# Optimization experiments

Hardware: AMD Instinct MI355X
Metric: run time of the kernel (lower is better)

## Reference

```python
import jax, jax.numpy as jnp
import numpy as np

B, S, DM, TD, H, HD = 2, 2048, 1024, 1024, 16, 64


def setup_inputs() -> dict:
    key = jax.random.key(0)
    k1, k2, k3, k4 = jax.random.split(key, 4)
    query = jax.random.normal(k1, (B, S, DM), dtype=jnp.float32)
    # fused QKV projection weight (nn.Linear weight layout: [out, in]) and output proj
    W_in = jax.random.normal(k2, (3 * TD, DM), dtype=jnp.float32) * 0.02
    W_out = jax.random.normal(k3, (DM, TD), dtype=jnp.float32) * 0.02
    # standard RoPE tables, broadcastable against [B, H, S, HD]
    inv_freq = 1.0 / (10000.0 ** (jnp.arange(0, HD, 2, dtype=jnp.float32) / HD))
    t = jnp.arange(S, dtype=jnp.float32)
    freqs = jnp.outer(t, inv_freq)                      # [S, HD/2]
    emb = jnp.concatenate([freqs, freqs], axis=-1)      # [S, HD]
    sin_q = jnp.sin(emb)[None, None]                    # [1,1,S,HD]
    cos_q = jnp.cos(emb)[None, None]
    # padding mask over keys: first length[b] positions valid (>= S/2 so no NaN rows)
    lengths = jax.random.randint(k4, (B,), S // 2, S + 1)
    attn_mask = jnp.arange(S)[None, :] < lengths[:, None]  # [B, S] bool
    return {"query": query, "W_in": W_in, "W_out": W_out,
            "sin_q": sin_q, "cos_q": cos_q, "attn_mask": attn_mask}


def _rotate_half(x):
    x1, x2 = jnp.split(x, 2, axis=-1)
    return jnp.concatenate([-x2, x1], axis=-1)


def reference(query, W_in, W_out, sin_q, cos_q, attn_mask):
    # fused QKV projection (proj_in, bias=False)
    qkv = query @ W_in.T                                # [B, S, 3*TD]
    q, k, v = jnp.split(qkv, 3, axis=-1)
    to_heads = lambda x: x.reshape(B, S, H, HD).transpose(0, 2, 1, 3)  # [B,H,S,HD]
    q, k, v = to_heads(q), to_heads(k), to_heads(v)
    # RoPE (prefix = 0 since sin covers full sequence)
    q = q * cos_q + _rotate_half(q) * sin_q
    k = k * cos_q + _rotate_half(k) * sin_q
    # SDPA with padding-mask bias + causal mask
    scale = 1.0 / jnp.sqrt(jnp.float32(HD))
    scores = jnp.einsum('bhqd,bhkd->bhqk', q, k) * scale  # [B,H,S,S]
    causal = jnp.arange(S)[:, None] >= jnp.arange(S)[None, :]  # [S, S]
    mask = attn_mask[:, None, None, :] & causal[None, None]    # [B,1,S,S]
    scores = jnp.where(mask, scores, -jnp.inf)
    attn = jax.nn.softmax(scores, axis=-1)
    out = jnp.einsum('bhqk,bhkd->bhqd', attn, v)        # [B,H,S,HD]
    out = out.transpose(0, 2, 1, 3).reshape(B, S, TD)
    return out @ W_out.T                                 # [B, S, DM]
```

## Files before the change

### kernel.cpp

```cpp
#include <hip/hip_runtime.h>
#include <hip/hip_bf16.h>

#define B_ 2
#define S_ 2048
#define DM_ 1024
#define TD_ 1024
#define H_ 16
#define HD_ 64

using bf16 = __hip_bfloat16;
typedef __attribute__((ext_vector_type(8))) short s8v;
typedef __attribute__((ext_vector_type(4))) float f4v;

__device__ __forceinline__ f4v mfma_bf16(s8v a, s8v b, f4v c) {
    return __builtin_amdgcn_mfma_f32_16x16x32_bf16(a, b, c, 0, 0, 0);
}

__device__ __forceinline__ unsigned cvt_pk_bf16(float a, float b) {
    unsigned r;
    asm("v_cvt_pk_bf16_f32 %0, %1, %2" : "=v"(r) : "v"(a), "v"(b));
    return r;
}
__device__ __forceinline__ int2 pack4bf(float a, float b, float c, float d) {
    int2 r;
    r.x = (int)cvt_pk_bf16(a, b);
    r.y = (int)cvt_pk_bf16(c, d);
    return r;
}

__device__ __forceinline__ bool detect_f32(const unsigned int* __restrict__ cosw) {
    return (cosw[0] & 0xFFFFu) == 0u;
}

__device__ __forceinline__ void gload_lds16(const bf16* g, void* l) {
    __builtin_amdgcn_global_load_lds(
        (const __attribute__((address_space(1))) unsigned int*)(const void*)g,
        (__attribute__((address_space(3))) unsigned int*)l,
        16, 0, 0);
}

#define NQ_  (B_ * S_ * DM_)
#define NWI_ (3 * TD_ * DM_)
#define NWO_ (DM_ * TD_)
#define NCVT_BLOCKS ((NQ_ + NWI_ + NWO_) / 2048)

__global__ __launch_bounds__(256)
void prep_all(const void* __restrict__ q, const void* __restrict__ wi,
              const void* __restrict__ wo, bf16* __restrict__ dst,
              const void* __restrict__ mask, int* __restrict__ lengths,
              const unsigned int* __restrict__ cosw) {
    const int bid = blockIdx.x;
    if (bid < NCVT_BLOCKS) {
        const bool f32 = detect_f32(cosw);
        int i = (bid * 256 + threadIdx.x) * 8;
        const void* src; int off;
        if (i < NQ_)              { src = q;  off = i; }
        else if (i < NQ_ + NWI_)  { src = wi; off = i - NQ_; }
        else                      { src = wo; off = i - NQ_ - NWI_; }
        if (f32) {
            const float* p = (const float*)src + off;
            float4 x = *reinterpret_cast<const float4*>(p);
            float4 y = *reinterpret_cast<const float4*>(p + 4);
            union { unsigned u[4]; int4 v; } t;
            t.u[0] = cvt_pk_bf16(x.x, x.y);
            t.u[1] = cvt_pk_bf16(x.z, x.w);
            t.u[2] = cvt_pk_bf16(y.x, y.y);
            t.u[3] = cvt_pk_bf16(y.z, y.w);
            *reinterpret_cast<int4*>(dst + i) = t.v;
        } else {
            *reinterpret_cast<int4*>(dst + i) =
                *reinterpret_cast<const int4*>((const bf16*)src + off);
        }
        return;
    }
    int b = bid - NCVT_BLOCKS;
    unsigned int w0 = ((const unsigned int*)mask)[0];
    int enc;
    if (w0 == 1u) enc = 0;
    else if (w0 == 0x01010101u) enc = 1;
    else if (w0 == 0x3F803F80u) enc = 2;
    else enc = 3;
    int cnt = 0;
    for (int s = threadIdx.x; s < S_; s += 256) {
        int i = b * S_ + s;
        bool v;
        if (enc == 0)      v = ((const int*)mask)[i] != 0;
        else if (enc == 1) v = ((const unsigned char*)mask)[i] != 0;
        else if (enc == 2) v = ((const unsigned short*)mask)[i] != 0;
        else               v = ((const float*)mask)[i] != 0.f;
        cnt += v ? 1 : 0;
    }
    __shared__ int red[256];
    red[threadIdx.x] = cnt;
    __syncthreads();
    for (int off = 128; off > 0; off >>= 1) {
        if (threadIdx.x < off) red[threadIdx.x] += red[threadIdx.x + off];
        __syncthreads();
    }
    if (threadIdx.x == 0) lengths[b] = red[0];
}

__global__ __launch_bounds__(256, 4)
void gemm_out(const bf16* __restrict__ A, const bf16* __restrict__ Bm,
              void* __restrict__ C, int M, int N, int K,
              int c_dyn, const unsigned int* __restrict__ cosw) {
    __shared__ bf16 lds_a[128 * 64];
    __shared__ bf16 lds_b[64 * 64];

    const bool cf32 = c_dyn && detect_f32(cosw);

    const int t = threadIdx.x;
    const int wave = t >> 6, lane = t & 63;
    const int quad = lane >> 4, l16 = lane & 15;
    const int wm = wave >> 1, wn = wave & 1;
    const int bid = blockIdx.x;
    const int c = bid & 7, g = bid >> 3;
    const int m0 = (c * 4 + (g & 3)) * 128;
    const int n0 = (g >> 2) * 64;
    const int wuni = __builtin_amdgcn_readfirstlane(wave);

    f4v acc[4][2];
    #pragma unroll
    for (int i = 0; i < 4; i++)
        #pragma unroll
        for (int j = 0; j < 2; j++)
            acc[i][j] = f4v{0.f, 0.f, 0.f, 0.f};

    for (int k0 = 0; k0 < K; k0 += 64) {
        __syncthreads();
        #pragma unroll
        for (int i = 0; i < 4; i++) {
            int ci = i * 256 + t;
            int row = ci >> 3;
            int csrc = (ci & 7) ^ (row & 7);
            gload_lds16(A + (size_t)(m0 + row) * K + k0 + csrc * 8,
                        (char*)lds_a + i * 4096 + wuni * 1024);
        }
        #pragma unroll
        for (int i = 0; i < 2; i++) {
            int ci = i * 256 + t;
            int row = ci >> 3;
            int csrc = (ci & 7) ^ (row & 7);
            gload_lds16(Bm + (size_t)(n0 + row) * K + k0 + csrc * 8,
                        (char*)lds_b + i * 4096 + wuni * 1024);
        }
        __syncthreads();

        #pragma unroll
        for (int kk = 0; kk < 2; kk++) {
            s8v afr[4], bfr[2];
            #pragma unroll
            for (int mb = 0; mb < 4; mb++) {
                int r = wm * 64 + mb * 16 + l16;
                int ch = (kk * 4 + quad) ^ (l16 & 7);
                afr[mb] = *reinterpret_cast<const s8v*>(&lds_a[r * 64 + ch * 8]);
            }
            #pragma unroll
            for (int nb = 0; nb < 2; nb++) {
                int r = wn * 32 + nb * 16 + l16;
                int ch = (kk * 4 + quad) ^ (l16 & 7);
                bfr[nb] = *reinterpret_cast<const s8v*>(&lds_b[r * 64 + ch * 8]);
            }
            #pragma unroll
            for (int mb = 0; mb < 4; mb++)
                #pragma unroll
                for (int nb = 0; nb < 2; nb++)
                    acc[mb][nb] = mfma_bf16(bfr[nb], afr[mb], acc[mb][nb]);
        }
    }

    #pragma unroll
    for (int mb = 0; mb < 4; mb++) {
        int m = m0 + wm * 64 + mb * 16 + l16;
        #pragma unroll
        for (int nb = 0; nb < 2; nb++) {
            int n = n0 + wn * 32 + nb * 16 + quad * 4;
            f4v v = acc[mb][nb];
            if (cf32) {
                *reinterpret_cast<f4v*>(&((float*)C)[(size_t)m * N + n]) = v;
            } else {
                *reinterpret_cast<int2*>(&((bf16*)C)[(size_t)m * N + n]) =
                    pack4bf(v[0], v[1], v[2], v[3]);
            }
        }
    }
}

__global__ __launch_bounds__(256, 3)
void gemm_qkv(const bf16* __restrict__ A, const bf16* __restrict__ Bm,
              bf16* __restrict__ Qh, bf16* __restrict__ Kt, bf16* __restrict__ Vt,
              const void* __restrict__ sin_t, const void* __restrict__ cos_t) {
    __shared__ bf16 lds_a[128 * 64];
    __shared__ bf16 lds_b[128 * 64];

    const int t = threadIdx.x;
    const int wave = t >> 6, lane = t & 63;
    const int quad = lane >> 4, l16 = lane & 15;
    const int wm = wave >> 1, wn = wave & 1;
    const int bid = blockIdx.x;
    const int c = bid & 7, g = bid >> 3;
    const int m0 = (c * 4 + (g & 3)) * 128;
    const int n0 = (g >> 2) * 128;
    const int wuni = __builtin_amdgcn_readfirstlane(wave);

    f4v acc[4][4];
    #pragma unroll
    for (int i = 0; i < 4; i++)
        #pragma unroll
        for (int j = 0; j < 4; j++)
            acc[i][j] = f4v{0.f, 0.f, 0.f, 0.f};

    for (int k0 = 0; k0 < 1024; k0 += 64) {
        __syncthreads();
        #pragma unroll
        for (int i = 0; i < 4; i++) {
            int ci = i * 256 + t;
            int row = ci >> 3;
            int csrc = (ci & 7) ^ (row & 7);
            gload_lds16(A + (size_t)(m0 + row) * 1024 + k0 + csrc * 8,
                        (char*)lds_a + i * 4096 + wuni * 1024);
            gload_lds16(Bm + (size_t)(n0 + row) * 1024 + k0 + csrc * 8,
                        (char*)lds_b + i * 4096 + wuni * 1024);
        }
        __syncthreads();

        #pragma unroll
        for (int kk = 0; kk < 2; kk++) {
            s8v afr[4], bfr[4];
            #pragma unroll
            for (int mb = 0; mb < 4; mb++) {
                int r = wm * 64 + mb * 16 + l16;
                int ch = (kk * 4 + quad) ^ (l16 & 7);
                afr[mb] = *reinterpret_cast<const s8v*>(&lds_a[r * 64 + ch * 8]);
            }
            #pragma unroll
            for (int nb = 0; nb < 4; nb++) {
                int r = wn * 64 + nb * 16 + l16;
                int ch = (kk * 4 + quad) ^ (l16 & 7);
                bfr[nb] = *reinterpret_cast<const s8v*>(&lds_b[r * 64 + ch * 8]);
            }
            #pragma unroll
            for (int mb = 0; mb < 4; mb++)
                #pragma unroll
                for (int nb = 0; nb < 4; nb++)
                    acc[mb][nb] = mfma_bf16(bfr[nb], afr[mb], acc[mb][nb]);
        }
    }

    const int region = n0 >> 10;
    if (region < 2) {
        const bool f32 = detect_f32((const unsigned int*)cos_t);
        #pragma unroll
        for (int mb = 0; mb < 4; mb++) {
            const int m = m0 + wm * 64 + mb * 16 + l16;
            const int b = m >> 11, s = m & 2047;
            #pragma unroll
            for (int nb = 0; nb < 4; nb++) {
                const int n = n0 + wn * 64 + nb * 16 + quad * 4;
                const int d = n & 63;
                const int h = (n >> 6) & 15;
                const float sgn = (nb < 2) ? -1.f : 1.f;
                f4v v  = acc[mb][nb];
                f4v vp = acc[mb][nb ^ 2];
                float cs[4], sn[4];
                if (f32) {
                    float4 c4 = *reinterpret_cast<const float4*>(
                        (const float*)cos_t + s * 64 + d);
                    float4 s4 = *reinterpret_cast<const float4*>(
                        (const float*)sin_t + s * 64 + d);
                    cs[0] = c4.x; cs[1] = c4.y; cs[2] = c4.z; cs[3] = c4.w;
                    sn[0] = s4.x; sn[1] = s4.y; sn[2] = s4.z; sn[3] = s4.w;
                } else {
                    const bf16* cp = (const bf16*)cos_t + s * 64 + d;
                    const bf16* sp = (const bf16*)sin_t + s * 64 + d;
                    #pragma unroll
                    for (int r = 0; r < 4; r++) {
                        cs[r] = __bfloat162float(cp[r]);
                        sn[r] = __bfloat162float(sp[r]);
                    }
                }
                float y[4];
                #pragma unroll
                for (int r = 0; r < 4; r++)
                    y[r] = v[r] * cs[r] + sgn * vp[r] * sn[r];
                if (region == 0) {
                    size_t o = ((size_t)(b * H_ + h) * S_ + s) * 64 + d;
                    *reinterpret_cast<int2*>(&Qh[o]) =
                        pack4bf(y[0] * 0.180336880f, y[1] * 0.180336880f,
                                y[2] * 0.180336880f, y[3] * 0.180336880f);
                } else {
                    size_t kt = ((size_t)(b * H_ + h) * 32 + (s >> 6)) * 4096;
                    int dp = ((((d >> 3) ^ (s & 7)) << 3) | (d & 7));
                    *reinterpret_cast<int2*>(&Kt[kt + (s & 63) * 64 + dp]) =
                        pack4bf(y[0], y[1], y[2], y[3]);
                }
            }
        }
    } else {
        __syncthreads();
        bf16* half_w = (wm == 0) ? lds_a : lds_b;
        #pragma unroll
        for (int mb = 0; mb < 4; mb++) {
            const int slr = mb * 16 + l16;
            #pragma unroll
            for (int nb = 0; nb < 4; nb++) {
                const int nl = wn * 64 + nb * 16 + quad * 4;
                f4v v = acc[mb][nb];
                int off = (((nl >> 3) ^ (slr & 7)) << 3) | (nl & 7);
                *reinterpret_cast<int2*>(&half_w[slr * 128 + off]) =
                    pack4bf(v[0], v[1], v[2], v[3]);
            }
        }
        __syncthreads();
        const int b  = m0 >> 11;
        const int h0 = (n0 - 2048) >> 6;
        const int r0 = t & 7;
        #pragma unroll
        for (int i = 0; i < 8; i++) {
            int id  = i * 256 + t;
            int kc  = id & 7;
            int d   = (id >> 3) & 63;
            int sbl = (id >> 9) & 1;
            int hh  = id >> 10;
            int cb  = (hh << 3) | (d >> 3);
            const short* half_r = reinterpret_cast<const short*>(
                sbl ? lds_b : lds_a);
            union { short s_[8]; int4 v4; } u;
            #pragma unroll
            for (int j = 0; j < 8; j++) {
                int e   = (j + r0) & 7;
                int slr = kc * 8 + e;
                u.s_[e] = half_r[slr * 128 + (((cb ^ e) << 3) | (d & 7))];
            }
            size_t tb = ((size_t)(b * H_ + h0 + hh) * 32 +
                         ((m0 & 2047) >> 6) + sbl) * 4096;
            *reinterpret_cast<int4*>(&Vt[tb + d * 64 + ((kc ^ (d & 7)) << 3)]) = u.v4;
        }
    }
}

__global__ __launch_bounds__(256)
void attn_fused(const bf16* __restrict__ Qh, const bf16* __restrict__ Kt,
                const bf16* __restrict__ Vt, const int* __restrict__ lengths,
                bf16* __restrict__ out) {
    __shared__ bf16 k_buf[2 * 4096];
    __shared__ bf16 v_buf[2 * 4096];
    __shared__ bf16 lds_p[4 * 16 * 72];

    const int t = threadIdx.x, wave = t >> 6, lane = t & 63;
    const int quad = lane >> 4, l16 = lane & 15;
    const int bid = blockIdx.x;
    const int slot = bid >> 3;
    const int bh = (bid & 7) * 4 + (slot >> 4);
    const int p = slot & 15;
    const int b = bh >> 4, h = bh & 15;

    const size_t hb = (size_t)bh * S_ * 64;
    const bf16* Ktp = Kt + (size_t)bh * 32 * 4096;
    const bf16* Vtp = Vt + (size_t)bh * 32 * 4096;
    const int wuni = __builtin_amdgcn_readfirstlane(wave);
    int len_raw = lengths[b];
    const int len_b = len_raw < 1 ? 1 : (len_raw > S_ ? S_ : len_raw);
    const int nkt_len = (len_b + 63) >> 6;

    #pragma unroll
    for (int pass = 0; pass < 2; pass++) {
        const int qb = pass ? (31 - p) : p;
        const int qbase = qb * 64;
        const int qrow_g = qbase + wave * 16 + l16;
        const int kmax = (qrow_g < len_b - 1) ? qrow_g : (len_b - 1);

        s8v qf[2];
        {
            const bf16* qptr = Qh + hb + (size_t)qrow_g * 64 + quad * 8;
            qf[0] = *reinterpret_cast<const s8v*>(qptr);
            qf[1] = *reinterpret_cast<const s8v*>(qptr + 32);
        }

        f4v o_acc[4];
        #pragma unroll
        for (int a = 0; a < 4; a++) o_acc[a] = f4v{0.f, 0.f, 0.f, 0.f};
        float l_sum = 0.f;

        const int nkt = (qb + 1) < nkt_len ? (qb + 1) : nkt_len;

        f4v s_prev[4];
        auto process_tile = [&](int pt, const bf16* vb) {
            const int pbase = pt * 64;
            const bool tail = (pt == qb) || (pbase + 64 > len_b);
            #pragma unroll
            for (int a = 0; a < 4; a++) {
                float e0[4];
                #pragma unroll
                for (int r = 0; r < 4; r++) {
                    float e = __builtin_amdgcn_exp2f(s_prev[a][r]);
                    if (tail) {
                        int key = pbase + a * 16 + quad * 4 + r;
                        e = (key <= kmax) ? e : 0.f;
                    }
                    e0[r] = e;
                    l_sum += e;
                }
                *reinterpret_cast<int2*>(
                    &lds_p[(wave * 16 + l16) * 72 + a * 16 + quad * 4]) =
                    pack4bf(e0[0], e0[1], e0[2], e0[3]);
            }
            asm volatile("s_waitcnt lgkmcnt(0)" ::: "memory");
            __builtin_amdgcn_s_setprio(1);
            #pragma unroll
            for (int kk = 0; kk < 2; kk++) {
                s8v pf = *reinterpret_cast<const s8v*>(
                    &lds_p[(wave * 16 + l16) * 72 + kk * 32 + quad * 8]);
                #pragma unroll
                for (int a = 0; a < 4; a++) {
                    int ch = (kk * 4 + quad) ^ (l16 & 7);
                    s8v vf = *reinterpret_cast<const s8v*>(
                        &vb[(a * 16 + l16) * 64 + ch * 8]);
                    o_acc[a] = mfma_bf16(vf, pf, o_acc[a]);
                }
            }
            __builtin_amdgcn_s_setprio(0);
        };

        #pragma unroll
        for (int i = 0; i < 2; i++) {
            int ci = i * 256 + t;
            gload_lds16(Ktp + ci * 8, (char*)k_buf + i * 4096 + wuni * 1024);
        }
        __syncthreads();

        for (int kt = 0; kt < nkt; kt++) {
            const int cur = kt & 1;
            {
                const bf16* vst = Vtp + (size_t)kt * 4096;
                #pragma unroll
                for (int i = 0; i < 2; i++) {
                    int ci = i * 256 + t;
                    gload_lds16(vst + ci * 8,
                                (char*)v_buf + cur * 8192 + i * 4096 + wuni * 1024);
                }
            }
            if (kt + 1 < nkt) {
                const bf16* kst = Ktp + (size_t)(kt + 1) * 4096;
                #pragma unroll
                for (int i = 0; i < 2; i++) {
                    int ci = i * 256 + t;
                    gload_lds16(kst + ci * 8,
                                (char*)k_buf + (cur ^ 1) * 8192 + i * 4096 + wuni * 1024);
                }
            }

            const bf16* kb = k_buf + cur * 4096;
            f4v s_acc[4];
            #pragma unroll
            for (int a = 0; a < 4; a++) s_acc[a] = f4v{0.f, 0.f, 0.f, 0.f};
            __builtin_amdgcn_s_setprio(1);
            #pragma unroll
            for (int kk = 0; kk < 2; kk++) {
                #pragma unroll
                for (int a = 0; a < 4; a++) {
                    int ch = (kk * 4 + quad) ^ (l16 & 7);
                    s8v kf = *reinterpret_cast<const s8v*>(
                        &kb[(a * 16 + l16) * 64 + ch * 8]);
                    s_acc[a] = mfma_bf16(kf, qf[kk], s_acc[a]);
                }
            }
            __builtin_amdgcn_s_setprio(0);

            if (kt > 0) process_tile(kt - 1, v_buf + ((kt - 1) & 1) * 4096);

            #pragma unroll
            for (int a = 0; a < 4; a++) s_prev[a] = s_acc[a];

            __syncthreads();
        }
        process_tile(nkt - 1, v_buf + ((nkt - 1) & 1) * 4096);

        l_sum += __shfl_xor(l_sum, 16);
        l_sum += __shfl_xor(l_sum, 32);
        float inv_l = 1.f / l_sum;
        size_t orow = ((size_t)(b * S_ + qrow_g)) * TD_ + h * 64;
        #pragma unroll
        for (int a = 0; a < 4; a++) {
            *reinterpret_cast<int2*>(&out[orow + a * 16 + quad * 4]) =
                pack4bf(o_acc[a][0] * inv_l, o_acc[a][1] * inv_l,
                        o_acc[a][2] * inv_l, o_acc[a][3] * inv_l);
        }
    }
}

extern "C" void kernel_launch(void* const* d_in, const int* in_sizes, int n_in,
                              void* d_out, int out_size, void* d_ws, size_t ws_size,
                              hipStream_t stream) {
    const void* query = d_in[0];
    const void* W_in  = d_in[1];
    const void* W_out = d_in[2];
    const void* sin_q = d_in[3];
    const void* cos_q = d_in[4];
    const void* mask  = d_in[5];
    const unsigned int* cosw = (const unsigned int*)cos_q;

    const size_t nQ  = NQ_;
    const size_t nWi = NWI_;
    const size_t nWo = NWO_;

    bf16* base = (bf16*)d_ws;
    bf16* attn = base;
    bf16* Vt   = base + (size_t)4096 * 1024;
    bf16* Qh   = base + (size_t)2 * 4096 * 1024;
    bf16* Kt   = Qh + nQ;
    bf16* qbf  = Kt + nQ;
    bf16* wibf = qbf + nQ;
    bf16* wobf = wibf + nWi;
    int* lengths = (int*)(wobf + nWo);

    prep_all<<<NCVT_BLOCKS + B_, 256, 0, stream>>>(
        query, W_in, W_out, qbf, mask, lengths, cosw);

    gemm_qkv<<<768, 256, 0, stream>>>(qbf, wibf, Qh, Kt, Vt, sin_q, cos_q);

    attn_fused<<<512, 256, 0, stream>>>(Qh, Kt, Vt, lengths, attn);

    gemm_out<<<512, 256, 0, stream>>>(attn, wobf, d_out, 4096, 1024, 1024, 1, cosw);
}
```

Measured before the change: 177.2 us.

## Triple-buffer K/V tiles with prefetch distance two and partial vmcnt waits

Replaces the double-buffered K/V staging in the attention kernel with three-slot ring buffers. K is now prefetched two tiles ahead and V one tile ahead. The full __syncthreads waits become s_waitcnt vmcnt(N) plus s_barrier, so loads still in flight can stay outstanding across the barrier. This aims to hide global-to-LDS latency better, at the cost of more LDS per block (possible occupancy loss), modulo-3 index arithmetic, and fragile vmcnt counting.

```diff
diff --git a/kernel.cpp b/kernel.cpp
--- a/kernel.cpp
+++ b/kernel.cpp
@@ -343,8 +343,8 @@
 void attn_fused(const bf16* __restrict__ Qh, const bf16* __restrict__ Kt,
                 const bf16* __restrict__ Vt, const int* __restrict__ lengths,
                 bf16* __restrict__ out) {
-    __shared__ bf16 k_buf[2 * 4096];
-    __shared__ bf16 v_buf[2 * 4096];
+    __shared__ bf16 k_buf[3 * 4096];
+    __shared__ bf16 v_buf[3 * 4096];
     __shared__ bf16 lds_p[4 * 16 * 72];
 
     const int t = threadIdx.x, wave = t >> 6, lane = t & 63;
@@ -366,8 +366,7 @@
     #pragma unroll
     for (int pass = 0; pass < 2; pass++) {
         const int qb = pass ? (31 - p) : p;
-        const int qbase = qb * 64;
-        const int qrow_g = qbase + wave * 16 + l16;
+        const int qrow_g = qb * 64 + wave * 16 + l16;
         const int kmax = (qrow_g < len_b - 1) ? qrow_g : (len_b - 1);
 
         s8v qf[2];
@@ -422,35 +421,46 @@
             __builtin_amdgcn_s_setprio(0);
         };
 
-        #pragma unroll
-        for (int i = 0; i < 2; i++) {
-            int ci = i * 256 + t;
-            gload_lds16(Ktp + ci * 8, (char*)k_buf + i * 4096 + wuni * 1024);
-        }
-        __syncthreads();
+        __syncthreads();
+
+        #pragma unroll
+        for (int i = 0; i < 2; i++)
+            gload_lds16(Ktp + (i * 256 + t) * 8,
+                        (char*)k_buf + i * 4096 + wuni * 1024);
+        #pragma unroll
+        for (int i = 0; i < 2; i++)
+            gload_lds16(Vtp + (i * 256 + t) * 8,
+                        (char*)v_buf + i * 4096 + wuni * 1024);
+        if (nkt > 1) {
+            const bf16* kst = Ktp + 4096;
+            #pragma unroll
+            for (int i = 0; i < 2; i++)
+                gload_lds16(kst + (i * 256 + t) * 8,
+                            (char*)k_buf + 8192 + i * 4096 + wuni * 1024);
+            asm volatile("s_waitcnt vmcnt(4)\n\ts_barrier" ::: "memory");
+        } else {
+            asm volatile("s_waitcnt vmcnt(2)\n\ts_barrier" ::: "memory");
+        }
 
         for (int kt = 0; kt < nkt; kt++) {
-            const int cur = kt & 1;
-            {
-                const bf16* vst = Vtp + (size_t)kt * 4096;
-                #pragma unroll
-                for (int i = 0; i < 2; i++) {
-                    int ci = i * 256 + t;
-                    gload_lds16(vst + ci * 8,
-                                (char*)v_buf + cur * 8192 + i * 4096 + wuni * 1024);
-                }
-            }
             if (kt + 1 < nkt) {
-                const bf16* kst = Ktp + (size_t)(kt + 1) * 4096;
-                #pragma unroll
-                for (int i = 0; i < 2; i++) {
-                    int ci = i * 256 + t;
-                    gload_lds16(kst + ci * 8,
-                                (char*)k_buf + (cur ^ 1) * 8192 + i * 4096 + wuni * 1024);
-                }
-            }
-
-            const bf16* kb = k_buf + cur * 4096;
+                const bf16* vst = Vtp + (size_t)(kt + 1) * 4096;
+                const int vb3 = (kt + 1) % 3;
+                #pragma unroll
+                for (int i = 0; i < 2; i++)
+                    gload_lds16(vst + (i * 256 + t) * 8,
+                                (char*)v_buf + vb3 * 8192 + i * 4096 + wuni * 1024);
+            }
+            if (kt + 2 < nkt) {
+                const bf16* kst = Ktp + (size_t)(kt + 2) * 4096;
+                const int kb3 = (kt + 2) % 3;
+                #pragma unroll
+                for (int i = 0; i < 2; i++)
+                    gload_lds16(kst + (i * 256 + t) * 8,
+                                (char*)k_buf + kb3 * 8192 + i * 4096 + wuni * 1024);
+            }
+
+            const bf16* kb = k_buf + (kt % 3) * 4096;
             f4v s_acc[4];
             #pragma unroll
             for (int a = 0; a < 4; a++) s_acc[a] = f4v{0.f, 0.f, 0.f, 0.f};
@@ -467,14 +477,20 @@
             }
             __builtin_amdgcn_s_setprio(0);
 
-            if (kt > 0) process_tile(kt - 1, v_buf + ((kt - 1) & 1) * 4096);
+            if (kt > 0) process_tile(kt - 1, v_buf + ((kt - 1) % 3) * 4096);
 
             #pragma unroll
             for (int a = 0; a < 4; a++) s_prev[a] = s_acc[a];
 
-            __syncthreads();
-        }
-        process_tile(nkt - 1, v_buf + ((nkt - 1) & 1) * 4096);
+            if (kt + 2 < nkt) {
+                asm volatile("s_waitcnt vmcnt(4)\n\ts_barrier" ::: "memory");
+            } else if (kt + 1 < nkt) {
+                asm volatile("s_waitcnt vmcnt(2)\n\ts_barrier" ::: "memory");
+            } else {
+                asm volatile("s_waitcnt vmcnt(0)\n\ts_barrier" ::: "memory");
+            }
+        }
+        process_tile(nkt - 1, v_buf + ((nkt - 1) % 3) * 4096);
 
         l_sum += __shfl_xor(l_sum, 16);
         l_sum += __shfl_xor(l_sum, 32);
```

Result: no change. 179.9 us (+1.5%).
